# Performance work log

Hardware: AMD Instinct MI355X
Metric: run time of the kernel (lower is better)

## Reference

```python
import jax, jax.numpy as jnp
import numpy as np

H = W = 28
NUM_COUNTS = 10  # iteration counts 0..9, one per logit of determine_n


def conv2d(x, w, b=None, pad=2):
    # x: [B,C,H,W], w: [O,I,5,5]
    y = jax.lax.conv_general_dilated(
        x, w, window_strides=(1, 1), padding=[(pad, pad), (pad, pad)],
        dimension_numbers=("NCHW", "OIHW", "NCHW"))
    if b is not None:
        y = y + b[None, :, None, None]
    return y


def maxpool3(x):
    # kernel 3, stride 3, valid: 28 -> 9
    return jax.lax.reduce_window(
        x, -jnp.inf, jax.lax.max,
        window_dimensions=(1, 1, 3, 3), window_strides=(1, 1, 3, 3),
        padding="VALID")


def setup_inputs() -> dict:
    key = jax.random.key(0)
    ks = jax.random.split(key, 8)
    B = 4096
    s = 0.1
    return {
        "x": jax.random.normal(ks[0], (B, H * W), dtype=jnp.float32),
        "w1": jax.random.normal(ks[1], (8, 1, 5, 5), dtype=jnp.float32) * s,
        "b1": jax.random.normal(ks[2], (8,), dtype=jnp.float32) * s,
        "w2": jax.random.normal(ks[3], (16, 8, 5, 5), dtype=jnp.float32) * s,
        "b2": jax.random.normal(ks[4], (16,), dtype=jnp.float32) * s,
        "fcw": jax.random.normal(ks[5], (10, 16 * 9 * 9), dtype=jnp.float32) * s,
        "fcb": jax.random.normal(ks[6], (10,), dtype=jnp.float32) * s,
        "iterw": jax.random.normal(ks[7], (1, 1, 5, 5), dtype=jnp.float32) * s,
    }


def reference(x, w1, b1, w2, b2, fcw, fcb, iterw):
    B = x.shape[0]
    xi = x.reshape(B, 1, H, W)
    # determine_n: CNN router producing 10 logits over iteration counts
    h = jax.nn.relu(conv2d(xi, w1, b1))
    h = jax.nn.relu(conv2d(h, w2, b2))
    h = maxpool3(h).reshape(B, -1)                      # [B, 1296]
    logits = h @ fcw.T + fcb                            # [B, 10]
    probs = jax.nn.softmax(logits, axis=-1)             # [B, 10]
    # smooth TmIter: expected value over f^n(base), n = 0..9
    def step(y, _):
        return conv2d(y, iterw, None), y
    _, ys = jax.lax.scan(step, xi, None, length=NUM_COUNTS)  # [10,B,1,28,28]
    out = jnp.einsum("bn,nbchw->bchw", probs, ys)
    return out.reshape(B, H, W)
```

## Files before the change

kernel.cpp:

```cpp
#include <hip/hip_runtime.h>
#include <hip/hip_bf16.h>
#include <math.h>
#include <float.h>

typedef __fp16 f16x8  __attribute__((ext_vector_type(8)));
typedef float  f32x16 __attribute__((ext_vector_type(16)));
typedef float  f32x4  __attribute__((ext_vector_type(4)));

#define DY_TAB 0xA524A509A502A540ULL
#define DX_TAB 0x446A444A44924924ULL

__global__ __launch_bounds__(256, 4) void k1_router(
    const float* __restrict__ xg,
    const float* __restrict__ w1g,
    const float* __restrict__ b1g,
    const float* __restrict__ w2g,
    const float* __restrict__ b2g,
    const float* __restrict__ fcwg,
    const float* __restrict__ fcbg,
    float* __restrict__ wsp)
{
    __shared__ __align__(16) char lds[28528];
    float*  spad   = (float*)(lds + 0);
    __fp16* sh1T   = (__fp16*)(lds + 4608);
    __fp16* sw2t   = (__fp16*)(lds + 21968);
    float*  pooled = (float*)(lds + 21968);
    float*  swred  = (float*)(lds + 28368);

    const int tid  = threadIdx.x;
    const int b    = blockIdx.x;
    const int lane = tid & 63;
    const int wid  = tid >> 6;

    f32x4 z4 = {0.f, 0.f, 0.f, 0.f};
    for (int i = tid; i < 92; i += 256) {
        int row, cu;
        if (i < 36) { int r = i / 9; cu = i - 9 * r; row = r < 2 ? r : 28 + r; }
        else        { int j = i - 36; row = 2 + (j >> 1); cu = (j & 1) << 3; }
        ((f32x4*)spad)[row * 9 + cu] = z4;
    }
    for (int i = tid; i < 1085; i += 256) ((f32x4*)sh1T)[i] = z4;
    for (int i = tid; i < 400; i += 256) {
        const int tap = i >> 4, ch = i & 15;
        f16x8 v;
        #pragma unroll
        for (int j = 0; j < 8; ++j) v[j] = (__fp16)w2g[ch * 200 + j * 25 + tap];
        *((f16x8*)(sw2t + i * 8)) = v;
    }
    const int yy = tid / 7, q = tid - yy * 7;
    if (tid < 196) {
        f32x4 v = *((const f32x4*)(xg + (size_t)b * 784 + yy * 28 + q * 4));
        *((f32x4*)(spad + (yy + 2) * 36 + q * 4 + 4)) = v;
    }
    __syncthreads();

    if (tid < 196) {
        float o[8][4];
        #pragma unroll
        for (int c = 0; c < 8; ++c) {
            const float bv = b1g[c];
            #pragma unroll
            for (int px = 0; px < 4; ++px) o[c][px] = bv;
        }
        #pragma unroll
        for (int r = 0; r < 5; ++r) {
            const float* rowp = spad + (yy + r) * 36 + q * 4;
            f32x4 a0 = ((const f32x4*)rowp)[0];
            f32x4 a1 = ((const f32x4*)rowp)[1];
            f32x4 a2 = ((const f32x4*)rowp)[2];
            float u[12] = {a0[0],a0[1],a0[2],a0[3], a1[0],a1[1],a1[2],a1[3],
                           a2[0],a2[1],a2[2],a2[3]};
            #pragma unroll
            for (int c = 0; c < 8; ++c)
                #pragma unroll
                for (int kx = 0; kx < 5; ++kx) {
                    const float w = w1g[c * 25 + r * 5 + kx];
                    #pragma unroll
                    for (int px = 0; px < 4; ++px)
                        o[c][px] = fmaf(u[2 + px + kx], w, o[c][px]);
                }
        }
        #pragma unroll
        for (int px = 0; px < 4; ++px) {
            f16x8 hv;
            #pragma unroll
            for (int c = 0; c < 8; ++c) hv[c] = (__fp16)fmaxf(o[c][px], 0.f);
            *((f16x8*)(sh1T + ((yy + 2) * 35 + (q * 4 + px + 2)) * 8)) = hv;
        }
    }
    const int lr = lane & 31;
    const int g2 = lane >> 5;
    int band = (lr * 57) >> 9; band = band > 2 ? 2 : band;
    const int dy = (int)((DY_TAB >> (2 * lr)) & 3ull);
    const int dx = (int)((DX_TAB >> (2 * lr)) & 3ull);
    const float biasv = (lr < 16) ? b2g[lr] : 0.f;

    f16x8 bfrag[13];
    int   toffB[13];
    #pragma unroll
    for (int s = 0; s < 13; ++s) {
        const int tap = 2 * s + g2;
        const int tapc = tap > 24 ? 24 : tap;
        f16x8 v = *((const f16x8*)(sw2t + (tapc * 16 + (lr & 15)) * 8));
        if (tap > 24 || lr >= 16) {
            #pragma unroll
            for (int j = 0; j < 8; ++j) v[j] = (__fp16)0.f;
        }
        bfrag[s] = v;
        const int ky = (tapc * 13) >> 6;
        const int kx = tapc - 5 * ky;
        toffB[s] = (ky * 35 + kx) * 16;
    }
    __syncthreads();

    auto tileBase = [&](int tile) -> const char* {
        const int cell = tile * 3 + band;
        const int cy = (cell * 57) >> 9, cx = cell - 9 * cy;
        return (const char*)sh1T + ((3 * cy + dy) * 35 + (3 * cx + dx)) * 16;
    };
    auto epi = [&](const f32x16& acc, int tile) {
        float mA, mB, mC;
        if (g2 == 0) {
            mA = fmaxf(fmaxf(fmaxf(acc[0],acc[1]),fmaxf(acc[2],acc[3])), acc[4]);
            mB = fmaxf(fmaxf(fmaxf(acc[5],acc[6]),acc[7]), fmaxf(acc[8],acc[9]));
            mC = fmaxf(fmaxf(fmaxf(acc[10],acc[11]),acc[12]), fmaxf(acc[13],acc[14]));
        } else {
            mA = fmaxf(fmaxf(acc[0],acc[1]),fmaxf(acc[2],acc[3]));
            mB = fmaxf(fmaxf(acc[4],acc[5]),fmaxf(acc[6],acc[7]));
            mC = fmaxf(fmaxf(acc[8],acc[9]),fmaxf(acc[10],acc[11]));
        }
        mA = fmaxf(mA, 0.f); mB = fmaxf(mB, 0.f); mC = fmaxf(mC, 0.f);
        mA = fmaxf(mA, __shfl_xor(mA, 32, 64));
        mB = fmaxf(mB, __shfl_xor(mB, 32, 64));
        mC = fmaxf(mC, __shfl_xor(mC, 32, 64));
        if (g2 == 0 && lr < 16) {
            pooled[lr * 81 + tile * 3 + 0] = mA;
            pooled[lr * 81 + tile * 3 + 1] = mB;
            pooled[lr * 81 + tile * 3 + 2] = mC;
        }
    };
    #pragma unroll 1
    for (int base = wid; base + 4 < 27; base += 8) {
        const char* a0 = tileBase(base);
        const char* a1 = tileBase(base + 4);
        f32x16 acc0, acc1;
        #pragma unroll
        for (int r = 0; r < 16; ++r) { acc0[r] = biasv; acc1[r] = biasv; }
        #pragma unroll
        for (int s = 0; s < 13; ++s) {
            f16x8 af0 = *((const f16x8*)(a0 + toffB[s]));
            f16x8 af1 = *((const f16x8*)(a1 + toffB[s]));
            acc0 = __builtin_amdgcn_mfma_f32_32x32x16_f16(af0, bfrag[s], acc0, 0, 0, 0);
            acc1 = __builtin_amdgcn_mfma_f32_32x32x16_f16(af1, bfrag[s], acc1, 0, 0, 0);
        }
        epi(acc0, base);
        epi(acc1, base + 4);
    }
    if (wid < 3) {
        const int tile = wid + 24;
        const char* a0 = tileBase(tile);
        f32x16 acc;
        #pragma unroll
        for (int r = 0; r < 16; ++r) acc[r] = biasv;
        #pragma unroll
        for (int s = 0; s < 13; ++s) {
            f16x8 af = *((const f16x8*)(a0 + toffB[s]));
            acc = __builtin_amdgcn_mfma_f32_32x32x16_f16(af, bfrag[s], acc, 0, 0, 0);
        }
        epi(acc, tile);
    }
    __syncthreads();

    {
        float part[10];
        #pragma unroll
        for (int j = 0; j < 10; ++j) part[j] = 0.f;
        for (int i4 = tid; i4 < 324; i4 += 256) {
            const f32x4 pv = ((const f32x4*)pooled)[i4];
            #pragma unroll
            for (int j = 0; j < 10; ++j) {
                const f32x4 fw = *((const f32x4*)(fcwg + j * 1296 + i4 * 4));
                part[j] = fmaf(pv[0], fw[0], part[j]);
                part[j] = fmaf(pv[1], fw[1], part[j]);
                part[j] = fmaf(pv[2], fw[2], part[j]);
                part[j] = fmaf(pv[3], fw[3], part[j]);
            }
        }
        #pragma unroll
        for (int j = 0; j < 10; ++j) {
            float v = part[j];
            #pragma unroll
            for (int off = 32; off > 0; off >>= 1) v += __shfl_down(v, off, 64);
            if (lane == 0) swred[wid * 10 + j] = v;
        }
    }
    __syncthreads();

    if (tid == 0) {
        float lg[10]; float mx = -FLT_MAX;
        #pragma unroll
        for (int j = 0; j < 10; ++j) {
            lg[j] = swred[j] + swred[10 + j] + swred[20 + j] + swred[30 + j] + fcbg[j];
            mx = fmaxf(mx, lg[j]);
        }
        float sum = 0.f; float e[10];
        #pragma unroll
        for (int j = 0; j < 10; ++j) { e[j] = expf(lg[j] - mx); sum += e[j]; }
        const float inv = 1.f / sum;
        #pragma unroll
        for (int j = 0; j < 10; ++j) wsp[(size_t)b * 16 + j] = e[j] * inv;
    }
}

__global__ __launch_bounds__(64, 4) void k2_scan(
    const float* __restrict__ xg,
    const float* __restrict__ iwg,
    const float* __restrict__ wsp,
    float* __restrict__ outg)
{
    __shared__ __align__(16) float arena[3456];
    float* spad = arena;
    float* bufA = arena + 1152;
    float* bufB = arena + 2304;

    const int tid = threadIdx.x;
    const int b   = blockIdx.x;

    f32x4 z4 = {0.f, 0.f, 0.f, 0.f};
    for (int i = tid; i < 864; i += 64) ((f32x4*)arena)[i] = z4;
    __syncthreads();

    for (int i = tid; i < 196; i += 64) {
        const int yy = i / 7, q = i - yy * 7;
        f32x4 v = *((const f32x4*)(xg + (size_t)b * 784 + yy * 28 + q * 4));
        *((f32x4*)(spad + (yy + 2) * 36 + q * 4 + 4)) = v;
    }
    __syncthreads();

    float iw[25];
    #pragma unroll
    for (int k = 0; k < 25; ++k) iw[k] = iwg[k];

    const int rp = tid / 7, qq = tid - rp * 7;
    const float p0 = wsp[(size_t)b * 16];
    float accv[16];
    #pragma unroll
    for (int i = 0; i < 16; ++i) accv[i] = 0.f;

    const float* cur = spad;
    float* nxt = bufA;
    #pragma unroll 1
    for (int n = 1; n <= 9; ++n) {
        const float pn = wsp[(size_t)b * 16 + n];
        if (tid < 49) {
            float v[4][4];
            #pragma unroll
            for (int rr = 0; rr < 4; ++rr)
                #pragma unroll
                for (int px = 0; px < 4; ++px) v[rr][px] = 0.f;
            #pragma unroll
            for (int r = 0; r < 8; ++r) {
                const float* rowp = cur + (4 * rp + r) * 36 + qq * 4;
                f32x4 a0 = ((const f32x4*)rowp)[0];
                f32x4 a1 = ((const f32x4*)rowp)[1];
                f32x4 a2 = ((const f32x4*)rowp)[2];
                float u[12] = {a0[0],a0[1],a0[2],a0[3], a1[0],a1[1],a1[2],a1[3],
                               a2[0],a2[1],a2[2],a2[3]};
                if (n == 1 && r >= 2 && r <= 5) {
                    #pragma unroll
                    for (int px = 0; px < 4; ++px)
                        accv[(r - 2) * 4 + px] = p0 * u[4 + px];
                }
                #pragma unroll
                for (int rr = 0; rr < 4; ++rr) {
                    if (rr <= r && r <= rr + 4) {
                        const int ky = r - rr;
                        #pragma unroll
                        for (int kx = 0; kx < 5; ++kx)
                            #pragma unroll
                            for (int px = 0; px < 4; ++px)
                                v[rr][px] = fmaf(u[2 + px + kx], iw[ky * 5 + kx], v[rr][px]);
                    }
                }
            }
            if (n < 9) {
                #pragma unroll
                for (int rr = 0; rr < 4; ++rr) {
                    f32x4 w = {v[rr][0], v[rr][1], v[rr][2], v[rr][3]};
                    *((f32x4*)(nxt + (4 * rp + rr + 2) * 36 + qq * 4 + 4)) = w;
                }
            }
            #pragma unroll
            for (int rr = 0; rr < 4; ++rr)
                #pragma unroll
                for (int px = 0; px < 4; ++px)
                    accv[rr * 4 + px] = fmaf(pn, v[rr][px], accv[rr * 4 + px]);
        }
        if (n < 9) __syncthreads();
        cur = nxt;
        nxt = (n & 1) ? bufB : bufA;
    }

    if (tid < 49) {
        #pragma unroll
        for (int rr = 0; rr < 4; ++rr) {
            f32x4 o = {accv[rr*4], accv[rr*4+1], accv[rr*4+2], accv[rr*4+3]};
            *((f32x4*)(outg + (size_t)b * 784 + (4 * rp + rr) * 28 + qq * 4)) = o;
        }
    }
}

extern "C" void kernel_launch(void* const* d_in, const int* in_sizes, int n_in,
                              void* d_out, int out_size, void* d_ws, size_t ws_size,
                              hipStream_t stream) {
    const float* x   = (const float*)d_in[0];
    const float* w1  = (const float*)d_in[1];
    const float* b1  = (const float*)d_in[2];
    const float* w2  = (const float*)d_in[3];
    const float* b2  = (const float*)d_in[4];
    const float* fcw = (const float*)d_in[5];
    const float* fcb = (const float*)d_in[6];
    const float* iw  = (const float*)d_in[7];
    float* out = (float*)d_out;
    float* wsp = (float*)d_ws;
    const int B = in_sizes[0] / 784;
    k1_router<<<B, 256, 0, stream>>>(x, w1, b1, w2, b2, fcw, fcb, wsp);
    k2_scan<<<B, 64, 0, stream>>>(x, iw, wsp, out);
}
```

Before: 114.2 us.

## Use packed fp16 dot2 for conv1 and iterative 5x5 conv

```diff
diff --git a/kernel.cpp b/kernel.cpp
--- a/kernel.cpp
+++ b/kernel.cpp
@@ -4,8 +4,25 @@
 #include <float.h>
 
 typedef __fp16 f16x8  __attribute__((ext_vector_type(8)));
+typedef __fp16 f16x2  __attribute__((ext_vector_type(2)));
 typedef float  f32x16 __attribute__((ext_vector_type(16)));
 typedef float  f32x4  __attribute__((ext_vector_type(4)));
+typedef unsigned int u32x4 __attribute__((ext_vector_type(4)));
+typedef unsigned int u32x2 __attribute__((ext_vector_type(2)));
+
+__device__ inline f16x2 as_h2(unsigned u) { union { unsigned x; f16x2 h; } c; c.x = u; return c.h; }
+__device__ inline unsigned pack2(float lo, float hi) {
+    union { f16x2 h; unsigned x; } c; c.h[0] = (__fp16)lo; c.h[1] = (__fp16)hi; return c.x;
+}
+__device__ inline float dot2f(unsigned a, unsigned b, float acc) {
+#if __has_builtin(__builtin_amdgcn_fdot2)
+    return __builtin_amdgcn_fdot2(as_h2(a), as_h2(b), acc, false);
+#else
+    f16x2 ah = as_h2(a), bh = as_h2(b);
+    return fmaf((float)ah[1], (float)bh[1], fmaf((float)ah[0], (float)bh[0], acc));
+#endif
+}
+#define ALIGN16(hi, lo) __builtin_amdgcn_alignbit((hi), (lo), 16)
 
 #define DY_TAB 0xA524A509A502A540ULL
 #define DX_TAB 0x446A444A44924924ULL
@@ -20,12 +37,13 @@
     const float* __restrict__ fcbg,
     float* __restrict__ wsp)
 {
-    __shared__ __align__(16) char lds[28528];
-    float*  spad   = (float*)(lds + 0);
-    __fp16* sh1T   = (__fp16*)(lds + 4608);
-    __fp16* sw2t   = (__fp16*)(lds + 21968);
-    float*  pooled = (float*)(lds + 21968);
-    float*  swred  = (float*)(lds + 28368);
+    __shared__ __align__(16) char lds[27120];
+    char*   spadh  = lds;
+    char*   wpk    = lds + 2560;
+    __fp16* sh1T   = (__fp16*)(lds + 3200);
+    __fp16* sw2t   = (__fp16*)(lds + 20560);
+    float*  pooled = (float*)(lds + 20560);
+    float*  swred  = (float*)(lds + 26960);
 
     const int tid  = threadIdx.x;
     const int b    = blockIdx.x;
@@ -33,12 +51,7 @@
     const int wid  = tid >> 6;
 
     f32x4 z4 = {0.f, 0.f, 0.f, 0.f};
-    for (int i = tid; i < 92; i += 256) {
-        int row, cu;
-        if (i < 36) { int r = i / 9; cu = i - 9 * r; row = r < 2 ? r : 28 + r; }
-        else        { int j = i - 36; row = 2 + (j >> 1); cu = (j & 1) << 3; }
-        ((f32x4*)spad)[row * 9 + cu] = z4;
-    }
+    for (int i = tid; i < 160; i += 256)  ((f32x4*)spadh)[i] = z4;
     for (int i = tid; i < 1085; i += 256) ((f32x4*)sh1T)[i] = z4;
     for (int i = tid; i < 400; i += 256) {
         const int tap = i >> 4, ch = i & 15;
@@ -47,10 +60,18 @@
         for (int j = 0; j < 8; ++j) v[j] = (__fp16)w2g[ch * 200 + j * 25 + tap];
         *((f16x8*)(sw2t + i * 8)) = v;
     }
+    if (tid < 40) {
+        const int r = tid >> 3, c = tid & 7;
+        const float* w = w1g + c * 25 + r * 5;
+        u32x4 W;
+        W.x = pack2(w[0], w[1]); W.y = pack2(w[2], w[3]); W.z = pack2(w[4], 0.f); W.w = 0u;
+        *((u32x4*)(wpk + tid * 16)) = W;
+    }
     const int yy = tid / 7, q = tid - yy * 7;
     if (tid < 196) {
         f32x4 v = *((const f32x4*)(xg + (size_t)b * 784 + yy * 28 + q * 4));
-        *((f32x4*)(spad + (yy + 2) * 36 + q * 4 + 4)) = v;
+        unsigned* dst = (unsigned*)(spadh + (yy + 2) * 80 + q * 8 + 4);
+        dst[0] = pack2(v[0], v[1]); dst[1] = pack2(v[2], v[3]);
     }
     __syncthreads();
 
@@ -64,21 +85,24 @@
         }
         #pragma unroll
         for (int r = 0; r < 5; ++r) {
-            const float* rowp = spad + (yy + r) * 36 + q * 4;
-            f32x4 a0 = ((const f32x4*)rowp)[0];
-            f32x4 a1 = ((const f32x4*)rowp)[1];
-            f32x4 a2 = ((const f32x4*)rowp)[2];
-            float u[12] = {a0[0],a0[1],a0[2],a0[3], a1[0],a1[1],a1[2],a1[3],
-                           a2[0],a2[1],a2[2],a2[3]};
-            #pragma unroll
-            for (int c = 0; c < 8; ++c)
-                #pragma unroll
-                for (int kx = 0; kx < 5; ++kx) {
-                    const float w = w1g[c * 25 + r * 5 + kx];
-                    #pragma unroll
-                    for (int px = 0; px < 4; ++px)
-                        o[c][px] = fmaf(u[2 + px + kx], w, o[c][px]);
+            const char* rowb = spadh + (yy + r) * 80 + q * 8;
+            u32x2 A = *((const u32x2*)rowb);
+            u32x2 B = *((const u32x2*)(rowb + 8));
+            unsigned C0 = *((const unsigned*)(rowb + 16));
+            unsigned P[8] = { A.x, ALIGN16(A.y, A.x), A.y, ALIGN16(B.x, A.y),
+                              B.x, ALIGN16(B.y, B.x), B.y, ALIGN16(C0,  B.y) };
+            #pragma unroll
+            for (int c = 0; c < 8; ++c) {
+                const u32x4 W = *((const u32x4*)(wpk + (r * 8 + c) * 16));
+                #pragma unroll
+                for (int px = 0; px < 4; ++px) {
+                    float t = o[c][px];
+                    t = dot2f(P[px],     W.x, t);
+                    t = dot2f(P[px + 2], W.y, t);
+                    t = dot2f(P[px + 4], W.z, t);
+                    o[c][px] = t;
                 }
+            }
         }
         #pragma unroll
         for (int px = 0; px < 4; ++px) {
@@ -218,37 +242,41 @@
     const float* __restrict__ wsp,
     float* __restrict__ outg)
 {
-    __shared__ __align__(16) float arena[3456];
-    float* spad = arena;
-    float* bufA = arena + 1152;
-    float* bufB = arena + 2304;
+    __shared__ __align__(16) char arena[5120];
+    char* bufA = arena;
+    char* bufB = arena + 2560;
 
     const int tid = threadIdx.x;
     const int b   = blockIdx.x;
 
     f32x4 z4 = {0.f, 0.f, 0.f, 0.f};
-    for (int i = tid; i < 864; i += 64) ((f32x4*)arena)[i] = z4;
+    for (int i = tid; i < 320; i += 64) ((f32x4*)arena)[i] = z4;
     __syncthreads();
 
     for (int i = tid; i < 196; i += 64) {
         const int yy = i / 7, q = i - yy * 7;
         f32x4 v = *((const f32x4*)(xg + (size_t)b * 784 + yy * 28 + q * 4));
-        *((f32x4*)(spad + (yy + 2) * 36 + q * 4 + 4)) = v;
-    }
-    __syncthreads();
-
-    float iw[25];
+        unsigned* dst = (unsigned*)(bufA + (yy + 2) * 80 + q * 8 + 4);
+        dst[0] = pack2(v[0], v[1]); dst[1] = pack2(v[2], v[3]);
+    }
+    __syncthreads();
+
+    unsigned wp[5][3];
     #pragma unroll
-    for (int k = 0; k < 25; ++k) iw[k] = iwg[k];
-
-    const int rp = tid / 7, qq = tid - rp * 7;
+    for (int r = 0; r < 5; ++r) {
+        wp[r][0] = pack2(iwg[r * 5 + 0], iwg[r * 5 + 1]);
+        wp[r][1] = pack2(iwg[r * 5 + 2], iwg[r * 5 + 3]);
+        wp[r][2] = pack2(iwg[r * 5 + 4], 0.f);
+    }
+
+    const int rq = tid / 7, qq = tid - rq * 7;
     const float p0 = wsp[(size_t)b * 16];
     float accv[16];
     #pragma unroll
     for (int i = 0; i < 16; ++i) accv[i] = 0.f;
 
-    const float* cur = spad;
-    float* nxt = bufA;
+    const char* cur = bufA;
+    char* nxt = bufB;
     #pragma unroll 1
     for (int n = 1; n <= 9; ++n) {
         const float pn = wsp[(size_t)b * 16 + n];
@@ -260,34 +288,40 @@
                 for (int px = 0; px < 4; ++px) v[rr][px] = 0.f;
             #pragma unroll
             for (int r = 0; r < 8; ++r) {
-                const float* rowp = cur + (4 * rp + r) * 36 + qq * 4;
-                f32x4 a0 = ((const f32x4*)rowp)[0];
-                f32x4 a1 = ((const f32x4*)rowp)[1];
-                f32x4 a2 = ((const f32x4*)rowp)[2];
-                float u[12] = {a0[0],a0[1],a0[2],a0[3], a1[0],a1[1],a1[2],a1[3],
-                               a2[0],a2[1],a2[2],a2[3]};
+                const char* rowb = cur + (4 * rq + r) * 80 + qq * 8;
+                u32x2 A = *((const u32x2*)rowb);
+                u32x2 B = *((const u32x2*)(rowb + 8));
+                unsigned C0 = *((const unsigned*)(rowb + 16));
+                unsigned P[8] = { A.x, ALIGN16(A.y, A.x), A.y, ALIGN16(B.x, A.y),
+                                  B.x, ALIGN16(B.y, B.x), B.y, ALIGN16(C0,  B.y) };
                 if (n == 1 && r >= 2 && r <= 5) {
-                    #pragma unroll
-                    for (int px = 0; px < 4; ++px)
-                        accv[(r - 2) * 4 + px] = p0 * u[4 + px];
+                    f16x2 t1 = as_h2(A.y), t2 = as_h2(B.x);
+                    accv[(r - 2) * 4 + 0] = p0 * (float)t1[0];
+                    accv[(r - 2) * 4 + 1] = p0 * (float)t1[1];
+                    accv[(r - 2) * 4 + 2] = p0 * (float)t2[0];
+                    accv[(r - 2) * 4 + 3] = p0 * (float)t2[1];
                 }
                 #pragma unroll
                 for (int rr = 0; rr < 4; ++rr) {
                     if (rr <= r && r <= rr + 4) {
                         const int ky = r - rr;
                         #pragma unroll
-                        for (int kx = 0; kx < 5; ++kx)
-                            #pragma unroll
-                            for (int px = 0; px < 4; ++px)
-                                v[rr][px] = fmaf(u[2 + px + kx], iw[ky * 5 + kx], v[rr][px]);
+                        for (int px = 0; px < 4; ++px) {
+                            float t = v[rr][px];
+                            t = dot2f(P[px],     wp[ky][0], t);
+                            t = dot2f(P[px + 2], wp[ky][1], t);
+                            t = dot2f(P[px + 4], wp[ky][2], t);
+                            v[rr][px] = t;
+                        }
                     }
                 }
             }
             if (n < 9) {
                 #pragma unroll
                 for (int rr = 0; rr < 4; ++rr) {
-                    f32x4 w = {v[rr][0], v[rr][1], v[rr][2], v[rr][3]};
-                    *((f32x4*)(nxt + (4 * rp + rr + 2) * 36 + qq * 4 + 4)) = w;
+                    unsigned* dst = (unsigned*)(nxt + (4 * rq + rr + 2) * 80 + qq * 8 + 4);
+                    dst[0] = pack2(v[rr][0], v[rr][1]);
+                    dst[1] = pack2(v[rr][2], v[rr][3]);
                 }
             }
             #pragma unroll
@@ -297,15 +331,14 @@
                     accv[rr * 4 + px] = fmaf(pn, v[rr][px], accv[rr * 4 + px]);
         }
         if (n < 9) __syncthreads();
-        cur = nxt;
-        nxt = (n & 1) ? bufB : bufA;
+        const char* t = cur; cur = nxt; nxt = (char*)t;
     }
 
     if (tid < 49) {
         #pragma unroll
         for (int rr = 0; rr < 4; ++rr) {
             f32x4 o = {accv[rr*4], accv[rr*4+1], accv[rr*4+2], accv[rr*4+3]};
-            *((f32x4*)(outg + (size_t)b * 784 + (4 * rp + rr) * 28 + qq * 4)) = o;
+            *((f32x4*)(outg + (size_t)b * 784 + (4 * rq + rr) * 28 + qq * 4)) = o;
         }
     }
 }
```

Result: slower. 117.2 us (+2.6%).
